# Kernel optimization log

Measured on AMD Instinct MI355X. Metric: run time of the kernel, lower is better.

The kernel has to match this reference:

```python
import jax, jax.numpy as jnp
import numpy as np

B, C, IMG, NP = 16, 3, 224, 14
PS = IMG // NP              # 16
D = 768                     # hidden_d (= C*PS*PS = input_d)
NH, L, OUT = 12, 12, 1000
DH = D // NH                # 64
MLP = 4 * D
S = NP * NP + 1             # 197 tokens (cls + patches)
EPS = 1e-5


def positional_embeddings(seq_len, dim):
    i = jnp.arange(seq_len, dtype=jnp.float32)[:, None]
    j = jnp.arange(dim, dtype=jnp.float32)[None, :]
    even = jnp.sin(i / 10000 ** (j / dim))
    odd = jnp.cos(i / 10000 ** ((j - 1) / dim))
    return jnp.where(jnp.arange(dim)[None, :] % 2 == 0, even, odd)


def patchify(images):
    # faithful to torch loop: patch = image[:, i*ps:(i+1)*ps, j*ps:(j+1)*ps].flatten()
    n = images.shape[0]
    x = images.reshape(n, C, NP, PS, NP, PS)
    x = x.transpose(0, 2, 4, 1, 3, 5)          # [n, NP, NP, C, PS, PS]
    return x.reshape(n, NP * NP, C * PS * PS)  # channel-major flatten per patch


def layernorm(x, g, b):
    m = jnp.mean(x, -1, keepdims=True)
    v = jnp.mean((x - m) ** 2, -1, keepdims=True)
    return (x - m) * jax.lax.rsqrt(v + EPS) * g + b


def setup_inputs() -> dict:
    key = jax.random.key(0)
    ks = iter(jax.random.split(key, 32))
    r = lambda shape, s=0.02: jax.random.normal(next(ks), shape, jnp.float32) * s
    inp = {
        "images": jax.random.normal(next(ks), (B, C, IMG, IMG), jnp.float32),
        "Wm": r((D, C * PS * PS)), "bm": r((D,)),
        "cls_tok": jax.random.uniform(next(ks), (1, D), jnp.float32),
        "pe": positional_embeddings(S, D),
        "g1": jnp.ones((L, D)), "beta1": jnp.zeros((L, D)),
        "Wq": r((L, NH, DH, D)), "bq": r((L, NH, DH)),
        "Wk": r((L, NH, DH, D)), "bk": r((L, NH, DH)),
        "Wv": r((L, NH, DH, D)), "bv": r((L, NH, DH)),
        "g2": jnp.ones((L, D)), "beta2": jnp.zeros((L, D)),
        "W1": r((L, MLP, D)), "b1": r((L, MLP)),
        "W2": r((L, D, MLP)), "b2": r((L, D)),
        "Wc": r((OUT, D)), "bc": r((OUT,)),
    }
    return inp


def vit_forward(images, Wm, bm, cls_tok, pe, g1, beta1, Wq, bq, Wk, bk, Wv, bv,
                g2, beta2, W1, b1, W2, b2, Wc, bc):
    n = images.shape[0]
    patches = patchify(images)                                    # [n, NP^2, input_d]
    tokens = patches @ Wm.T + bm                                  # [n, NP^2, D]
    cls = jnp.broadcast_to(cls_tok[None], (n, 1, D))
    out = jnp.concatenate([cls, tokens], axis=1) + pe             # [n, S, D]
    scale = 1.0 / jnp.sqrt(jnp.float32(DH))
    for l in range(L):
        x = layernorm(out, g1[l], beta1[l])
        # per-head Linear on FULL token (use_linear_mapping=True)
        q = jnp.einsum('bsd,hed->bhse', x, Wq[l]) + bq[l][None, :, None, :]
        k = jnp.einsum('bsd,hed->bhse', x, Wk[l]) + bk[l][None, :, None, :]
        v = jnp.einsum('bsd,hed->bhse', x, Wv[l]) + bv[l][None, :, None, :]
        att = jax.nn.softmax(jnp.einsum('bhse,bhte->bhst', q, k) * scale, axis=-1)
        o = jnp.einsum('bhst,bhte->bhse', att, v)                 # [n, H, S, DH]
        o = o.transpose(0, 2, 1, 3).reshape(n, S, D)              # hstack heads
        out = out + o
        y = layernorm(out, g2[l], beta2[l])
        h = jax.nn.gelu(y @ W1[l].T + b1[l], approximate=False)
        out = out + h @ W2[l].T + b2[l]
    pooled = out[:, 0]                                            # cls token
    return jax.nn.softmax(pooled @ Wc.T + bc, axis=-1)


def reference(images, Wm, bm, cls_tok, pe, g1, beta1, Wq, bq, Wk, bk, Wv, bv,
              g2, beta2, W1, b1, W2, b2, Wc, bc):
    return vit_forward(images, Wm, bm, cls_tok, pe, g1, beta1, Wq, bq, Wk, bk,
                       Wv, bv, g2, beta2, W1, b1, W2, b2, Wc, bc)
```

## Files before the change

### kernel.cpp

```cpp
#include <hip/hip_runtime.h>
#include <hip/hip_bf16.h>
#include <math.h>

typedef __hip_bfloat16 bf16;
typedef unsigned short ushort_t;
typedef short bf16x8 __attribute__((ext_vector_type(8)));
typedef float f32x4 __attribute__((ext_vector_type(4)));

static constexpr int BATCH = 16;
static constexpr int SEQ   = 197;
static constexpr int NHEAD = 12;
static constexpr int NMLP  = 3072;
static constexpr int NLAYER= 12;
static constexpr int NCLS  = 1000;
static constexpr int NPATCHES = 196;
static constexpr int MPAD  = 3200;

__device__ __forceinline__ ushort_t f2bu(float x) {
    bf16 v = __float2bfloat16(x);
    return *(ushort_t*)&v;
}

__device__ __forceinline__ void load_lds16(const void* g, void* l) {
    __builtin_amdgcn_global_load_lds(
        (const __attribute__((address_space(1))) void*)g,
        (__attribute__((address_space(3))) void*)l, 16, 0, 0);
}

__global__ __launch_bounds__(256) void mfma_gemm(
    const ushort_t* __restrict__ A, const ushort_t* __restrict__ B,
    const float* __restrict__ bias, float* __restrict__ Cf,
    bf16* __restrict__ Cb, int M, int N, int K, int mode)
{
    __shared__ ushort_t As[2][128 * 32];
    __shared__ ushort_t Bs[2][128 * 32];

    const int t  = threadIdx.x;
    const int m0 = blockIdx.y * 128;
    const int n0 = blockIdx.x * 128;

    const int srow = t >> 2;
    const int sp   = (t & 3) ^ ((srow >> 1) & 3);
    const int skp  = sp * 8;

    const int wave = t >> 6;
    const int lane = t & 63;
    const int wm   = (wave >> 1) * 64;
    const int wn   = (wave & 1) * 64;
    const int quad = lane >> 4;
    const int l16  = lane & 15;

    f32x4 acc[4][4] = {};

    const ushort_t* gA0 = A + (size_t)(m0 + srow) * K + skp;
    const ushort_t* gA1 = A + (size_t)(m0 + 64 + srow) * K + ((t & 3) ^ (((srow + 64) >> 1) & 3)) * 8;
    const ushort_t* gB0 = B + (size_t)(n0 + srow) * K + skp;
    const ushort_t* gB1 = B + (size_t)(n0 + 64 + srow) * K + ((t & 3) ^ (((srow + 64) >> 1) & 3)) * 8;
    const int t8 = t * 8;

    load_lds16(gA0, &As[0][t8]);
    load_lds16(gA1, &As[0][t8 + 2048]);
    load_lds16(gB0, &Bs[0][t8]);
    load_lds16(gB1, &Bs[0][t8 + 2048]);
    __syncthreads();

    int cur = 0;
    for (int k0 = 0; k0 < K; k0 += 32) {
        if (k0 + 32 < K) {
            const int nb = cur ^ 1;
            const int kn = k0 + 32;
            load_lds16(gA0 + kn, &As[nb][t8]);
            load_lds16(gA1 + kn, &As[nb][t8 + 2048]);
            load_lds16(gB0 + kn, &Bs[nb][t8]);
            load_lds16(gB1 + kn, &Bs[nb][t8 + 2048]);
        }

        bf16x8 af[4], bfr[4];
        #pragma unroll
        for (int i = 0; i < 4; ++i) {
            int row = wm + i * 16 + l16;
            int s = quad ^ ((row >> 1) & 3);
            af[i] = *(const bf16x8*)&As[cur][row * 32 + s * 8];
        }
        #pragma unroll
        for (int j = 0; j < 4; ++j) {
            int row = wn + j * 16 + l16;
            int s = quad ^ ((row >> 1) & 3);
            bfr[j] = *(const bf16x8*)&Bs[cur][row * 32 + s * 8];
        }
        #pragma unroll
        for (int i = 0; i < 4; ++i)
            #pragma unroll
            for (int j = 0; j < 4; ++j)
                acc[i][j] = __builtin_amdgcn_mfma_f32_16x16x32_bf16(
                    af[i], bfr[j], acc[i][j], 0, 0, 0);

        __syncthreads();
        cur ^= 1;
    }

    #pragma unroll
    for (int i = 0; i < 4; ++i) {
        int mrow = m0 + wm + i * 16 + quad * 4;
        #pragma unroll
        for (int j = 0; j < 4; ++j) {
            int col = n0 + wn + j * 16 + l16;
            float bv = bias ? bias[col] : 0.0f;
            #pragma unroll
            for (int r = 0; r < 4; ++r) {
                int m = mrow + r;
                if (m >= M) continue;
                float v = acc[i][j][r] + bv;
                size_t idx = (size_t)m * N + col;
                if (mode == 1) {
                    v = 0.5f * v * (1.0f + erff(v * 0.70710678118654752f));
                    Cb[idx] = __float2bfloat16(v);
                } else if (mode == 2) {
                    Cf[idx] += v;
                } else {
                    Cf[idx] = v;
                }
            }
        }
    }
}

__global__ void f2b_kernel(const float* __restrict__ src, bf16* __restrict__ dst, int n)
{
    int i4 = (blockIdx.x * 256 + threadIdx.x) * 4;
    for (; i4 < n; i4 += gridDim.x * 1024) {
        float4 v = *(const float4*)(src + i4);
        dst[i4 + 0] = __float2bfloat16(v.x);
        dst[i4 + 1] = __float2bfloat16(v.y);
        dst[i4 + 2] = __float2bfloat16(v.z);
        dst[i4 + 3] = __float2bfloat16(v.w);
    }
}

static constexpr int QKV_ELEMS = 3 * 768 * 768;
static constexpr int W1_ELEMS  = 3072 * 768;
static constexpr int CONV_VECS = (QKV_ELEMS + 2 * W1_ELEMS) / 4;
static constexpr int BIAS_VECS = 2304 / 4;

__global__ void convert_layer_kernel(
    const float* __restrict__ Wq, const float* __restrict__ Wk,
    const float* __restrict__ Wv, const float* __restrict__ W1,
    const float* __restrict__ W2, const float* __restrict__ bq,
    const float* __restrict__ bk, const float* __restrict__ bv,
    bf16* __restrict__ wqkv, bf16* __restrict__ w1b, bf16* __restrict__ w2b,
    float* __restrict__ bqkv)
{
    int idx = blockIdx.x * 256 + threadIdx.x;
    if (idx < BIAS_VECS) {
        int j = idx * 4;
        #pragma unroll
        for (int i = 0; i < 4; ++i) {
            int jj = j + i;
            float v = (jj < 768) ? bq[jj] : (jj < 1536) ? bk[jj - 768] : bv[jj - 1536];
            bqkv[jj] = v;
        }
    }
    int w = idx - BIAS_VECS;
    if (w < 0 || w >= CONV_VECS) return;
    const float* src;
    bf16* dst;
    int e;
    if (w < QKV_ELEMS / 4) {
        e = w * 4;
        int tsel = e / (768 * 768);
        int off = e - tsel * 768 * 768;
        src = (tsel == 0 ? Wq : tsel == 1 ? Wk : Wv) + off;
        dst = wqkv + tsel * 768 * 768 + off;
    } else if (w < QKV_ELEMS / 4 + W1_ELEMS / 4) {
        e = (w - QKV_ELEMS / 4) * 4;
        src = W1 + e;
        dst = w1b + e;
    } else {
        e = (w - QKV_ELEMS / 4 - W1_ELEMS / 4) * 4;
        src = W2 + e;
        dst = w2b + e;
    }
    float4 v = *(const float4*)src;
    dst[0] = __float2bfloat16(v.x);
    dst[1] = __float2bfloat16(v.y);
    dst[2] = __float2bfloat16(v.z);
    dst[3] = __float2bfloat16(v.w);
}

__global__ void patchify_kernel(const float* __restrict__ images,
                                bf16* __restrict__ patches, int total)
{
    int idx = blockIdx.x * 256 + threadIdx.x;
    if (idx >= total) return;
    int kidx = idx % 768;
    int p = (idx / 768) % NPATCHES;
    int b = idx / (768 * NPATCHES);
    int c  = kidx >> 8;
    int rem = kidx & 255;
    int iy = rem >> 4, ix = rem & 15;
    int py = p / 14, px = p % 14;
    size_t src = (((size_t)(b * 3 + c) * 224) + py * 16 + iy) * 224 + px * 16 + ix;
    patches[idx] = __float2bfloat16(images[src]);
}

__global__ void assemble_kernel(const float* __restrict__ tokens,
                                const float* __restrict__ cls,
                                const float* __restrict__ pe,
                                float* __restrict__ out, int total)
{
    int idx = blockIdx.x * 256 + threadIdx.x;
    if (idx >= total) return;
    int d = idx % 768;
    int s = (idx / 768) % SEQ;
    int b = idx / (768 * SEQ);
    float v = (s == 0) ? cls[d]
                       : tokens[((size_t)b * NPATCHES + (s - 1)) * 768 + d];
    out[idx] = v + pe[(size_t)s * 768 + d];
}

__global__ __launch_bounds__(256) void ln_kernel(const float* __restrict__ inp,
                                                 const float* __restrict__ g,
                                                 const float* __restrict__ beta,
                                                 bf16* __restrict__ xout)
{
    int r = blockIdx.x;
    const float* rowp = inp + (size_t)r * 768;
    float vals[3];
    float s = 0.f, s2 = 0.f;
    #pragma unroll
    for (int i = 0; i < 3; ++i) {
        float v = rowp[threadIdx.x + 256 * i];
        vals[i] = v; s += v; s2 += v * v;
    }
    __shared__ float rs[256], rs2[256];
    rs[threadIdx.x] = s; rs2[threadIdx.x] = s2;
    __syncthreads();
    for (int st = 128; st; st >>= 1) {
        if (threadIdx.x < st) {
            rs[threadIdx.x]  += rs[threadIdx.x + st];
            rs2[threadIdx.x] += rs2[threadIdx.x + st];
        }
        __syncthreads();
    }
    float mean = rs[0] * (1.0f / 768.0f);
    float var  = rs2[0] * (1.0f / 768.0f) - mean * mean;
    float rstd = rsqrtf(var + 1e-5f);
    #pragma unroll
    for (int i = 0; i < 3; ++i) {
        int d = threadIdx.x + 256 * i;
        xout[(size_t)r * 768 + d] =
            __float2bfloat16((vals[i] - mean) * rstd * g[d] + beta[d]);
    }
}

static constexpr int ATTN_LDS = (224 * 72 + 64 * 232 + 4 * 16 * 232) * 2;

__global__ __launch_bounds__(256) void attn_mfma_kernel(
    const float* __restrict__ qkv, float* __restrict__ out)
{
    extern __shared__ ushort_t smem[];
    ushort_t* Ks = smem;
    ushort_t* Vt = smem + 224 * 72;
    ushort_t* Ps = Vt + 64 * 232;

    const int bh = blockIdx.x;
    const int b = bh / NHEAD, h = bh % NHEAD;
    const int t = threadIdx.x;
    const int wave = t >> 6, lane = t & 63;
    const int quad = lane >> 4, l16 = lane & 15;

    for (int i = t; i < 224 * 16; i += 256) {
        int tr = i >> 4, e4 = (i & 15) << 2;
        float4 kv = {0.f, 0.f, 0.f, 0.f}, vv = {0.f, 0.f, 0.f, 0.f};
        if (tr < SEQ) {
            const float* base = qkv + (size_t)(b * SEQ + tr) * 2304 + h * 64 + e4;
            kv = *(const float4*)(base + 768);
            vv = *(const float4*)(base + 1536);
        }
        ushort_t kp[4] = {f2bu(kv.x), f2bu(kv.y), f2bu(kv.z), f2bu(kv.w)};
        *(uint2*)&Ks[tr * 72 + e4] = *(const uint2*)kp;
        Vt[(e4 + 0) * 232 + tr] = f2bu(vv.x);
        Vt[(e4 + 1) * 232 + tr] = f2bu(vv.y);
        Vt[(e4 + 2) * 232 + tr] = f2bu(vv.z);
        Vt[(e4 + 3) * 232 + tr] = f2bu(vv.w);
    }
    __syncthreads();

    bf16* pw = (bf16*)(Ps + wave * 16 * 232);

    for (int qt = wave; qt < 13; qt += 4) {
        const int q0 = qt * 16;

        bf16x8 qf[2];
        #pragma unroll
        for (int c = 0; c < 2; ++c) {
            const float* qp = qkv + (size_t)(b * SEQ + q0 + l16) * 2304
                            + h * 64 + c * 32 + quad * 8;
            float4 a = *(const float4*)qp;
            float4 b2 = *(const float4*)(qp + 4);
            qf[c][0] = (short)f2bu(a.x);  qf[c][1] = (short)f2bu(a.y);
            qf[c][2] = (short)f2bu(a.z);  qf[c][3] = (short)f2bu(a.w);
            qf[c][4] = (short)f2bu(b2.x); qf[c][5] = (short)f2bu(b2.y);
            qf[c][6] = (short)f2bu(b2.z); qf[c][7] = (short)f2bu(b2.w);
        }

        f32x4 sc[14] = {};
        #pragma unroll
        for (int tt = 0; tt < 14; ++tt) {
            #pragma unroll
            for (int c = 0; c < 2; ++c) {
                bf16x8 kf = *(const bf16x8*)&Ks[(tt * 16 + l16) * 72 + c * 32 + quad * 8];
                sc[tt] = __builtin_amdgcn_mfma_f32_16x16x32_bf16(qf[c], kf, sc[tt], 0, 0, 0);
            }
        }

        f32x4 m4;
        #pragma unroll
        for (int r = 0; r < 4; ++r) m4[r] = -3.4e38f;
        #pragma unroll
        for (int tt = 0; tt < 14; ++tt) {
            int tg = tt * 16 + l16;
            #pragma unroll
            for (int r = 0; r < 4; ++r) {
                sc[tt][r] = (tg < SEQ) ? sc[tt][r] * 0.125f : -1e30f;
                m4[r] = fmaxf(m4[r], sc[tt][r]);
            }
        }
        #pragma unroll
        for (int off = 1; off < 16; off <<= 1)
            #pragma unroll
            for (int r = 0; r < 4; ++r)
                m4[r] = fmaxf(m4[r], __shfl_xor(m4[r], off));

        f32x4 l4 = {};
        #pragma unroll
        for (int tt = 0; tt < 14; ++tt)
            #pragma unroll
            for (int r = 0; r < 4; ++r) {
                float p = __expf(sc[tt][r] - m4[r]);
                sc[tt][r] = p;
                l4[r] += p;
            }
        #pragma unroll
        for (int off = 1; off < 16; off <<= 1)
            #pragma unroll
            for (int r = 0; r < 4; ++r)
                l4[r] += __shfl_xor(l4[r], off);

        #pragma unroll
        for (int tt = 0; tt < 14; ++tt)
            #pragma unroll
            for (int r = 0; r < 4; ++r)
                pw[(quad * 4 + r) * 232 + tt * 16 + l16] = __float2bfloat16(sc[tt][r]);

        f32x4 oa[4] = {};
        #pragma unroll
        for (int c = 0; c < 7; ++c) {
            bf16x8 pf = *(const bf16x8*)&((ushort_t*)pw)[l16 * 232 + c * 32 + quad * 8];
            #pragma unroll
            for (int nt = 0; nt < 4; ++nt) {
                bf16x8 vf = *(const bf16x8*)&Vt[(nt * 16 + l16) * 232 + c * 32 + quad * 8];
                oa[nt] = __builtin_amdgcn_mfma_f32_16x16x32_bf16(pf, vf, oa[nt], 0, 0, 0);
            }
        }

        #pragma unroll
        for (int r = 0; r < 4; ++r) {
            int q = q0 + quad * 4 + r;
            if (q >= SEQ) continue;
            float rl = 1.0f / l4[r];
            float* orow = out + (size_t)(b * SEQ + q) * 768 + h * 64;
            #pragma unroll
            for (int nt = 0; nt < 4; ++nt)
                orow[nt * 16 + l16] += oa[nt][r] * rl;
        }
    }
}

__global__ __launch_bounds__(256) void cls_logits_kernel(
    const float* __restrict__ out, const float* __restrict__ Wc,
    const float* __restrict__ bc, float* __restrict__ logits)
{
    int b = blockIdx.y;
    int j = blockIdx.x * 256 + threadIdx.x;
    __shared__ float pooled[768];
    for (int d = threadIdx.x; d < 768; d += 256)
        pooled[d] = out[(size_t)b * SEQ * 768 + d];
    __syncthreads();
    if (j >= NCLS) return;
    const float* wr = Wc + (size_t)j * 768;
    float acc = 0.f;
    for (int d = 0; d < 768; ++d) acc += pooled[d] * wr[d];
    logits[b * NCLS + j] = acc + bc[j];
}

__global__ __launch_bounds__(256) void cls_softmax_kernel(
    const float* __restrict__ logits, float* __restrict__ dout)
{
    int b = blockIdx.x;
    __shared__ float red[256];
    const float* lg = logits + b * NCLS;

    float m = -3.4e38f;
    for (int j = threadIdx.x; j < NCLS; j += 256) m = fmaxf(m, lg[j]);
    red[threadIdx.x] = m; __syncthreads();
    for (int st = 128; st; st >>= 1) {
        if (threadIdx.x < st) red[threadIdx.x] = fmaxf(red[threadIdx.x], red[threadIdx.x + st]);
        __syncthreads();
    }
    m = red[0]; __syncthreads();

    float ssum = 0.f;
    for (int j = threadIdx.x; j < NCLS; j += 256) ssum += __expf(lg[j] - m);
    red[threadIdx.x] = ssum; __syncthreads();
    for (int st = 128; st; st >>= 1) {
        if (threadIdx.x < st) red[threadIdx.x] += red[threadIdx.x + st];
        __syncthreads();
    }
    float inv = 1.0f / red[0];
    __syncthreads();

    for (int j = threadIdx.x; j < NCLS; j += 256)
        dout[(size_t)b * NCLS + j] = __expf(lg[j] - m) * inv;
}

extern "C" void kernel_launch(void* const* d_in, const int* in_sizes, int n_in,
                              void* d_out, int out_size, void* d_ws, size_t ws_size,
                              hipStream_t stream)
{
    const float* images  = (const float*)d_in[0];
    const float* Wm      = (const float*)d_in[1];
    const float* bm      = (const float*)d_in[2];
    const float* cls_tok = (const float*)d_in[3];
    const float* pe      = (const float*)d_in[4];
    const float* g1      = (const float*)d_in[5];
    const float* beta1   = (const float*)d_in[6];
    const float* Wq      = (const float*)d_in[7];
    const float* bq      = (const float*)d_in[8];
    const float* Wk      = (const float*)d_in[9];
    const float* bk      = (const float*)d_in[10];
    const float* Wv      = (const float*)d_in[11];
    const float* bv      = (const float*)d_in[12];
    const float* g2      = (const float*)d_in[13];
    const float* beta2   = (const float*)d_in[14];
    const float* W1      = (const float*)d_in[15];
    const float* b1      = (const float*)d_in[16];
    const float* W2      = (const float*)d_in[17];
    const float* b2      = (const float*)d_in[18];
    const float* Wc      = (const float*)d_in[19];
    const float* bc      = (const float*)d_in[20];
    float* outp = (float*)d_out;

    const int M  = BATCH * SEQ;
    const int MP = BATCH * NPATCHES;

    char* ws = (char*)d_ws;
    float* out  = (float*)ws; ws += (size_t)MPAD * 768 * 4;
    bf16*  xb   = (bf16*) ws; ws += (size_t)MPAD * 768 * 2;
    float* qkv  = (float*)ws; ws += (size_t)MPAD * 2304 * 4;
    bf16*  h    = (bf16*) ws; ws += (size_t)MPAD * 3072 * 2;
    bf16*  wqkv = (bf16*) ws; ws += (size_t)2304 * 768 * 2;
    bf16*  w1b  = (bf16*) ws; ws += (size_t)3072 * 768 * 2;
    bf16*  w2b  = (bf16*) ws; ws += (size_t)768 * 3072 * 2;
    float* bqkv = (float*)ws; ws += 2304 * 4;
    bf16*  wmb  = (bf16*) ws; ws += (size_t)768 * 768 * 2;
    float* logits = (float*)ws; ws += (size_t)BATCH * NCLS * 4;
    bf16*  patches = (bf16*)h;
    float* tokens  = (float*)((char*)h + (size_t)MPAD * 768 * 2);

    hipFuncSetAttribute((const void*)attn_mfma_kernel,
                        hipFuncAttributeMaxDynamicSharedMemorySize, ATTN_LDS);

    f2b_kernel<<<576, 256, 0, stream>>>(Wm, wmb, 768 * 768);
    int tot_p = MP * 768;
    patchify_kernel<<<(tot_p + 255) / 256, 256, 0, stream>>>(images, patches, tot_p);
    mfma_gemm<<<dim3(768 / 128, (MP + 127) / 128), 256, 0, stream>>>(
        (const ushort_t*)patches, (const ushort_t*)wmb, bm, tokens, nullptr,
        MP, 768, 768, 0);
    int tot_a = M * 768;
    assemble_kernel<<<(tot_a + 255) / 256, 256, 0, stream>>>(tokens, cls_tok, pe, out, tot_a);

    const int MB = (M + 127) / 128;
    const int conv_blocks = (CONV_VECS + BIAS_VECS + 255) / 256;

    for (int l = 0; l < NLAYER; ++l) {
        convert_layer_kernel<<<conv_blocks, 256, 0, stream>>>(
            Wq + (size_t)l * 768 * 768, Wk + (size_t)l * 768 * 768,
            Wv + (size_t)l * 768 * 768, W1 + (size_t)l * NMLP * 768,
            W2 + (size_t)l * 768 * NMLP, bq + l * 768, bk + l * 768, bv + l * 768,
            wqkv, w1b, w2b, bqkv);

        ln_kernel<<<M, 256, 0, stream>>>(out, g1 + l * 768, beta1 + l * 768, xb);
        mfma_gemm<<<dim3(2304 / 128, MB), 256, 0, stream>>>(
            (const ushort_t*)xb, (const ushort_t*)wqkv, bqkv, qkv, nullptr,
            M, 2304, 768, 0);
        attn_mfma_kernel<<<BATCH * NHEAD, 256, ATTN_LDS, stream>>>(qkv, out);
        ln_kernel<<<M, 256, 0, stream>>>(out, g2 + l * 768, beta2 + l * 768, xb);
        mfma_gemm<<<dim3(NMLP / 128, MB), 256, 0, stream>>>(
            (const ushort_t*)xb, (const ushort_t*)w1b, b1 + l * NMLP, nullptr, h,
            M, NMLP, 768, 1);
        mfma_gemm<<<dim3(768 / 128, MB), 256, 0, stream>>>(
            (const ushort_t*)h, (const ushort_t*)w2b, b2 + l * 768, out, nullptr,
            M, 768, NMLP, 2);
    }

    cls_logits_kernel<<<dim3(4, BATCH), 256, 0, stream>>>(out, Wc, bc, logits);
    cls_softmax_kernel<<<BATCH, 256, 0, stream>>>(logits, outp);
}
```

Measured before the change: 2.745 ms.

## Double GEMM K-tile to 64 and remap workgroups across XCDs

The MFMA GEMM now stages 64-wide K slices per iteration instead of 32, with a matching 8-way XOR swizzle for LDS reads. This halves the number of barriers and loop iterations per tile. Workgroup indices are also remapped so that consecutive tiles land on the same XCD, which should improve L2 reuse. In exchange, LDS use doubles to 64KB per block, which may lower occupancy, and K must be a multiple of 64.

```diff
diff --git a/kernel.cpp b/kernel.cpp
--- a/kernel.cpp
+++ b/kernel.cpp
@@ -32,16 +32,23 @@
     const float* __restrict__ bias, float* __restrict__ Cf,
     bf16* __restrict__ Cb, int M, int N, int K, int mode)
 {
-    __shared__ ushort_t As[2][128 * 32];
-    __shared__ ushort_t Bs[2][128 * 32];
-
-    const int t  = threadIdx.x;
-    const int m0 = blockIdx.y * 128;
-    const int n0 = blockIdx.x * 128;
-
-    const int srow = t >> 2;
-    const int sp   = (t & 3) ^ ((srow >> 1) & 3);
-    const int skp  = sp * 8;
+    __shared__ ushort_t As[2][128 * 64];
+    __shared__ ushort_t Bs[2][128 * 64];
+
+    const int t = threadIdx.x;
+
+    const int nbx  = gridDim.x;
+    const int nwg  = nbx * gridDim.y;
+    const int orig = blockIdx.y * nbx + blockIdx.x;
+    const int xcd  = orig & 7;
+    const int loc  = orig >> 3;
+    const int qq   = nwg >> 3, rr = nwg & 7;
+    const int wg   = (xcd < rr ? xcd * (qq + 1) : rr * (qq + 1) + (xcd - rr) * qq) + loc;
+    const int m0   = (wg / nbx) * 128;
+    const int n0   = (wg % nbx) * 128;
+
+    const int srow = t >> 3;
+    const int sw   = ((t & 7) ^ (srow & 7)) * 8;
 
     const int wave = t >> 6;
     const int lane = t & 63;
@@ -52,48 +59,55 @@
 
     f32x4 acc[4][4] = {};
 
-    const ushort_t* gA0 = A + (size_t)(m0 + srow) * K + skp;
-    const ushort_t* gA1 = A + (size_t)(m0 + 64 + srow) * K + ((t & 3) ^ (((srow + 64) >> 1) & 3)) * 8;
-    const ushort_t* gB0 = B + (size_t)(n0 + srow) * K + skp;
-    const ushort_t* gB1 = B + (size_t)(n0 + 64 + srow) * K + ((t & 3) ^ (((srow + 64) >> 1) & 3)) * 8;
+    const ushort_t* gA[4];
+    const ushort_t* gB[4];
+    #pragma unroll
+    for (int p = 0; p < 4; ++p) {
+        gA[p] = A + (size_t)(m0 + p * 32 + srow) * K + sw;
+        gB[p] = B + (size_t)(n0 + p * 32 + srow) * K + sw;
+    }
     const int t8 = t * 8;
 
-    load_lds16(gA0, &As[0][t8]);
-    load_lds16(gA1, &As[0][t8 + 2048]);
-    load_lds16(gB0, &Bs[0][t8]);
-    load_lds16(gB1, &Bs[0][t8 + 2048]);
+    #pragma unroll
+    for (int p = 0; p < 4; ++p) {
+        load_lds16(gA[p], &As[0][p * 2048 + t8]);
+        load_lds16(gB[p], &Bs[0][p * 2048 + t8]);
+    }
     __syncthreads();
 
     int cur = 0;
-    for (int k0 = 0; k0 < K; k0 += 32) {
-        if (k0 + 32 < K) {
+    for (int k0 = 0; k0 < K; k0 += 64) {
+        if (k0 + 64 < K) {
             const int nb = cur ^ 1;
-            const int kn = k0 + 32;
-            load_lds16(gA0 + kn, &As[nb][t8]);
-            load_lds16(gA1 + kn, &As[nb][t8 + 2048]);
-            load_lds16(gB0 + kn, &Bs[nb][t8]);
-            load_lds16(gB1 + kn, &Bs[nb][t8 + 2048]);
-        }
-
-        bf16x8 af[4], bfr[4];
-        #pragma unroll
-        for (int i = 0; i < 4; ++i) {
-            int row = wm + i * 16 + l16;
-            int s = quad ^ ((row >> 1) & 3);
-            af[i] = *(const bf16x8*)&As[cur][row * 32 + s * 8];
-        }
-        #pragma unroll
-        for (int j = 0; j < 4; ++j) {
-            int row = wn + j * 16 + l16;
-            int s = quad ^ ((row >> 1) & 3);
-            bfr[j] = *(const bf16x8*)&Bs[cur][row * 32 + s * 8];
-        }
-        #pragma unroll
-        for (int i = 0; i < 4; ++i)
-            #pragma unroll
-            for (int j = 0; j < 4; ++j)
-                acc[i][j] = __builtin_amdgcn_mfma_f32_16x16x32_bf16(
-                    af[i], bfr[j], acc[i][j], 0, 0, 0);
+            const int kn = k0 + 64;
+            #pragma unroll
+            for (int p = 0; p < 4; ++p) {
+                load_lds16(gA[p] + kn, &As[nb][p * 2048 + t8]);
+                load_lds16(gB[p] + kn, &Bs[nb][p * 2048 + t8]);
+            }
+        }
+
+        #pragma unroll
+        for (int kk = 0; kk < 2; ++kk) {
+            bf16x8 af[4], bfr[4];
+            const int g = kk * 4 + quad;
+            #pragma unroll
+            for (int i = 0; i < 4; ++i) {
+                int row = wm + i * 16 + l16;
+                af[i] = *(const bf16x8*)&As[cur][row * 64 + (g ^ (row & 7)) * 8];
+            }
+            #pragma unroll
+            for (int j = 0; j < 4; ++j) {
+                int row = wn + j * 16 + l16;
+                bfr[j] = *(const bf16x8*)&Bs[cur][row * 64 + (g ^ (row & 7)) * 8];
+            }
+            #pragma unroll
+            for (int i = 0; i < 4; ++i)
+                #pragma unroll
+                for (int j = 0; j < 4; ++j)
+                    acc[i][j] = __builtin_amdgcn_mfma_f32_16x16x32_bf16(
+                        af[i], bfr[j], acc[i][j], 0, 0, 0);
+        }
 
         __syncthreads();
         cur ^= 1;
```

Result: slower. 2.835 ms (+3.3%).
